# Performance work log

Hardware: AMD Instinct MI355X
Metric: run time of the kernel (lower is better)

Reference implementation:

```python
import jax, jax.numpy as jnp
import numpy as np

NUM_CLASSES = 20
EPS = 1e-10


def setup_inputs() -> dict:
    key = jax.random.key(0)
    k1, k2 = jax.random.split(key)
    shape = (2, 128, 256, 256)
    prediction = jax.random.randint(k1, shape, 0, NUM_CLASSES, dtype=jnp.int32)
    target = jax.random.randint(k2, shape, 0, NUM_CLASSES, dtype=jnp.int32)
    return {"prediction": prediction, "target": target}


def reference(prediction, target):
    C = NUM_CLASSES
    pred = prediction.reshape(-1)
    tgt = target.reshape(-1)
    # Per-class voxel counts in a single histogram pass each.
    pred_cnt = jnp.bincount(pred, length=C).astype(jnp.float32)  # tp + fp per class
    tgt_cnt = jnp.bincount(tgt, length=C).astype(jnp.float32)    # tp + fn per class
    # tp: voxels where pred == tgt, binned by class (mismatches routed to bin C).
    tp = jnp.bincount(jnp.where(pred == tgt, pred, C), length=C + 1)[:C].astype(jnp.float32)
    # dsc = 2tp / (2tp + fp + fn + eps); fp = pred_cnt - tp, fn = tgt_cnt - tp.
    # Classes absent from both tensors give 0/eps = 0, matching the original's
    # skip-then-zero behavior.
    dscs = 2.0 * tp / (pred_cnt + tgt_cnt + EPS)
    return jnp.mean(dscs[1:])
```

## Files before the change

### kernel.cpp

```cpp
#include <hip/hip_runtime.h>

#define NC 20
#define THREADS 256
#define BLOCKS 2048
#define GRAN 8
#define EPSF 1e-10f

typedef unsigned long long u64;
typedef unsigned int u32;

#define PART_OFF 64
#define WS_NEEDED (256 + 30 * BLOCKS * 4)

static __device__ __forceinline__ void pair_update(int p, int t,
                                                   u64& np, u64& nt, u64& ne)
{
    u64 ip = 1ull << (3 * p);
    u64 it = 1ull << (3 * t);
    np += ip;
    nt += it;
    ne += (p == t) ? ip : 0ull;
}

__global__ __launch_bounds__(THREADS) void dice_slice(
    const int* __restrict__ pred, const int* __restrict__ tgt,
    u32* __restrict__ part)
{
    constexpr u64 M = 0x01C71C71C71C71C7ull;
    __shared__ u32 swave[4][30];
    const int tid = threadIdx.x;
    const int g   = blockIdx.x * THREADS + tid;
    const int S   = BLOCKS * THREADS;
    const int4* p4 = (const int4*)pred;
    const int4* t4 = (const int4*)tgt;

    u64 aeP=0, aoP=0, aeT=0, aoT=0, aeE=0, aoE=0;

    #pragma unroll
    for (int k = 0; k < GRAN; ++k) {
        int4 P = p4[g + k * S];
        int4 T = t4[g + k * S];
        u64 np = 0, nt = 0, ne = 0;
        pair_update(P.x, T.x, np, nt, ne);
        pair_update(P.y, T.y, np, nt, ne);
        pair_update(P.z, T.z, np, nt, ne);
        pair_update(P.w, T.w, np, nt, ne);
        aeP += np & M;        aoP += (np >> 3) & M;
        aeT += nt & M;        aoT += (nt >> 3) & M;
        aeE += ne & M;        aoE += (ne >> 3) & M;
    }

    const int wid  = tid >> 6;
    const int lane = tid & 63;
    #pragma unroll
    for (int j = 0; j < 10; ++j) {
        const int sh = 6 * j;
        u32 sP = (u32)((aeP >> sh) & 63) | ((u32)((aoP >> sh) & 63) << 16);
        u32 sT = (u32)((aeT >> sh) & 63) | ((u32)((aoT >> sh) & 63) << 16);
        u32 sE = (u32)((aeE >> sh) & 63) | ((u32)((aoE >> sh) & 63) << 16);
        #pragma unroll
        for (int d = 32; d >= 1; d >>= 1) {
            sP += __shfl_down(sP, d, 64);
            sT += __shfl_down(sT, d, 64);
            sE += __shfl_down(sE, d, 64);
        }
        if (lane == 0) {
            swave[wid][j]      = sP;
            swave[wid][10 + j] = sT;
            swave[wid][20 + j] = sE;
        }
    }
    __syncthreads();

    if (tid < 30) {
        u32 s = swave[0][tid] + swave[1][tid] + swave[2][tid] + swave[3][tid];
        part[tid * BLOCKS + blockIdx.x] = s;
    }
}

__global__ __launch_bounds__(THREADS) void dice_reduce(
    const u32* __restrict__ part, u32* __restrict__ gc)
{
    __shared__ u32 sw[2][4];
    const int j    = blockIdx.x;
    const int tid  = threadIdx.x;
    const int wid  = tid >> 6;
    const int lane = tid & 63;
    u32 lo = 0, hi = 0;
    #pragma unroll
    for (int k = 0; k < BLOCKS / THREADS; ++k) {
        u32 v = part[j * BLOCKS + tid + k * THREADS];
        lo += v & 0xFFFFu;
        hi += v >> 16;
    }
    #pragma unroll
    for (int d = 32; d >= 1; d >>= 1) {
        lo += __shfl_down(lo, d, 64);
        hi += __shfl_down(hi, d, 64);
    }
    if (lane == 0) { sw[0][wid] = lo; sw[1][wid] = hi; }
    __syncthreads();
    if (tid == 0) {
        lo = sw[0][0] + sw[0][1] + sw[0][2] + sw[0][3];
        hi = sw[1][0] + sw[1][1] + sw[1][2] + sw[1][3];
        const int hist = j / 10;
        const int k2   = j % 10;
        gc[hist * NC + 2 * k2]     = lo;
        gc[hist * NC + 2 * k2 + 1] = hi;
    }
}

__global__ __launch_bounds__(THREADS) void dice_joint(
    const int* __restrict__ pred, const int* __restrict__ tgt,
    u32* __restrict__ gc, long long n4)
{
    __shared__ u32 h[4 * NC * NC];
    const int tid = threadIdx.x;
    for (int k = tid; k < 4 * NC * NC; k += THREADS) h[k] = 0u;
    __syncthreads();
    u32* hw = &h[(tid >> 6) * NC * NC];
    const int4* p4 = (const int4*)pred;
    const int4* t4 = (const int4*)tgt;
    const long long stride = (long long)2048 * THREADS;
    for (long long i = (long long)blockIdx.x * THREADS + tid; i < n4; i += stride) {
        int4 P = p4[i];
        int4 T = t4[i];
        atomicAdd(&hw[P.x * NC + T.x], 1u);
        atomicAdd(&hw[P.y * NC + T.y], 1u);
        atomicAdd(&hw[P.z * NC + T.z], 1u);
        atomicAdd(&hw[P.w * NC + T.w], 1u);
    }
    __syncthreads();
    for (int k = tid; k < NC * NC; k += THREADS)
        h[k] = h[k] + h[NC*NC + k] + h[2*NC*NC + k] + h[3*NC*NC + k];
    __syncthreads();
    if (tid < 3 * (NC - 1)) {
        const int which = tid / (NC - 1);
        const int c     = tid % (NC - 1) + 1;
        u32 s = 0;
        if (which == 0)      { for (int t = 0; t < NC; ++t) s += h[c * NC + t]; }
        else if (which == 1) { for (int p = 0; p < NC; ++p) s += h[p * NC + c]; }
        else                 { s = h[c * NC + c]; }
        atomicAdd(&gc[which * NC + c], s);
    }
}

__global__ void dice_final(const u32* __restrict__ gc, float* __restrict__ out)
{
    const int c = threadIdx.x;
    float contrib = 0.0f;
    if (c >= 1 && c < NC) {
        float pc = (float)gc[c];
        float tc = (float)gc[NC + c];
        float tp = (float)gc[2 * NC + c];
        contrib = 2.0f * tp / (pc + tc + EPSF);
    }
    #pragma unroll
    for (int d = 32; d >= 1; d >>= 1) contrib += __shfl_down(contrib, d, 64);
    if (c == 0) out[0] = contrib * (1.0f / 19.0f);
}

extern "C" void kernel_launch(void* const* d_in, const int* in_sizes, int n_in,
                              void* d_out, int out_size, void* d_ws, size_t ws_size,
                              hipStream_t stream) {
    const int* pred = (const int*)d_in[0];
    const int* tgt  = (const int*)d_in[1];
    u32* gc   = (u32*)d_ws;
    u32* part = (u32*)d_ws + PART_OFF;

    const int n  = in_sizes[0];
    const int n4 = n >> 2;

    if (n4 == BLOCKS * THREADS * GRAN && ws_size >= (size_t)WS_NEEDED) {
        dice_slice<<<BLOCKS, THREADS, 0, stream>>>(pred, tgt, part);
        dice_reduce<<<30, THREADS, 0, stream>>>(part, gc);
    } else {
        hipMemsetAsync(d_ws, 0, 3 * NC * sizeof(u32), stream);
        dice_joint<<<2048, THREADS, 0, stream>>>(pred, tgt, gc, (long long)n4);
    }
    dice_final<<<1, 64, 0, stream>>>(gc, (float*)d_out);
}
```

Before: 39.55 us.

## Prefetch all granules via inline asm loads and fuse reduce with final kernel

The slice kernel now issues all 16 vector loads up front with inline global_load_dwordx4 and consumes each granule after a matching s_waitcnt, so memory latency overlaps with the bit-packed counting. The separate 30-block reduce kernel and the final dice kernel are merged into a single 1024-thread block that reduces the partials and computes the mean dice. This removes one kernel launch and the global round-trip through the workspace. The hand-written waitcnt counts depend on the compiler not issuing other vector memory ops in between, which is fragile.

```diff
diff --git a/kernel.cpp b/kernel.cpp
--- a/kernel.cpp
+++ b/kernel.cpp
@@ -8,6 +8,7 @@
 
 typedef unsigned long long u64;
 typedef unsigned int u32;
+typedef int v4i __attribute__((ext_vector_type(4)));
 
 #define PART_OFF 64
 #define WS_NEEDED (256 + 30 * BLOCKS * 4)
@@ -29,26 +30,39 @@
     constexpr u64 M = 0x01C71C71C71C71C7ull;
     __shared__ u32 swave[4][30];
     const int tid = threadIdx.x;
-    const int g   = blockIdx.x * THREADS + tid;
-    const int S   = BLOCKS * THREADS;
-    const int4* p4 = (const int4*)pred;
-    const int4* t4 = (const int4*)tgt;
-
-    u64 aeP=0, aoP=0, aeT=0, aoT=0, aeE=0, aoE=0;
-
+    const long long g = (long long)blockIdx.x * THREADS + tid;
+    const u64 SB = (u64)BLOCKS * THREADS * 16ull;
+
+    u64 baseP = (u64)pred + (u64)g * 16ull;
+    u64 baseT = (u64)tgt  + (u64)g * 16ull;
+
+    v4i P[GRAN], T[GRAN];
     #pragma unroll
     for (int k = 0; k < GRAN; ++k) {
-        int4 P = p4[g + k * S];
-        int4 T = t4[g + k * S];
-        u64 np = 0, nt = 0, ne = 0;
-        pair_update(P.x, T.x, np, nt, ne);
-        pair_update(P.y, T.y, np, nt, ne);
-        pair_update(P.z, T.z, np, nt, ne);
-        pair_update(P.w, T.w, np, nt, ne);
-        aeP += np & M;        aoP += (np >> 3) & M;
-        aeT += nt & M;        aoT += (nt >> 3) & M;
-        aeE += ne & M;        aoE += (ne >> 3) & M;
-    }
+        asm volatile("global_load_dwordx4 %0, %2, off\n\t"
+                     "global_load_dwordx4 %1, %3, off"
+                     : "=&v"(P[k]), "=&v"(T[k])
+                     : "v"(baseP + (u64)k * SB), "v"(baseT + (u64)k * SB));
+    }
+
+    u64 aeP=0, aoP=0, aeT=0, aoT=0, aeE=0, aoE=0;
+
+#define GRANULE(K, W)                                                          \
+    do {                                                                       \
+        asm volatile("s_waitcnt vmcnt(" #W ")" : "+v"(P[K]), "+v"(T[K]));      \
+        u64 np = 0, nt = 0, ne = 0;       \
+        pair_update(P[K].x, T[K].x, np, nt, ne);                               \
+        pair_update(P[K].y, T[K].y, np, nt, ne);                               \
+        pair_update(P[K].z, T[K].z, np, nt, ne);                               \
+        pair_update(P[K].w, T[K].w, np, nt, ne);                               \
+        aeP += np & M;        aoP += (np >> 3) & M;                            \
+        aeT += nt & M;        aoT += (nt >> 3) & M;                            \
+        aeE += ne & M;        aoE += (ne >> 3) & M;                            \
+    } while (0)
+
+    GRANULE(0, 14); GRANULE(1, 12); GRANULE(2, 10); GRANULE(3, 8);
+    GRANULE(4, 6);  GRANULE(5, 4);  GRANULE(6, 2);  GRANULE(7, 0);
+#undef GRANULE
 
     const int wid  = tid >> 6;
     const int lane = tid & 63;
@@ -78,35 +92,46 @@
     }
 }
 
-__global__ __launch_bounds__(THREADS) void dice_reduce(
-    const u32* __restrict__ part, u32* __restrict__ gc)
-{
-    __shared__ u32 sw[2][4];
-    const int j    = blockIdx.x;
-    const int tid  = threadIdx.x;
-    const int wid  = tid >> 6;
-    const int lane = tid & 63;
-    u32 lo = 0, hi = 0;
-    #pragma unroll
-    for (int k = 0; k < BLOCKS / THREADS; ++k) {
-        u32 v = part[j * BLOCKS + tid + k * THREADS];
-        lo += v & 0xFFFFu;
-        hi += v >> 16;
-    }
-    #pragma unroll
-    for (int d = 32; d >= 1; d >>= 1) {
-        lo += __shfl_down(lo, d, 64);
-        hi += __shfl_down(hi, d, 64);
-    }
-    if (lane == 0) { sw[0][wid] = lo; sw[1][wid] = hi; }
-    __syncthreads();
-    if (tid == 0) {
-        lo = sw[0][0] + sw[0][1] + sw[0][2] + sw[0][3];
-        hi = sw[1][0] + sw[1][1] + sw[1][2] + sw[1][3];
-        const int hist = j / 10;
-        const int k2   = j % 10;
-        gc[hist * NC + 2 * k2]     = lo;
-        gc[hist * NC + 2 * k2 + 1] = hi;
+__global__ __launch_bounds__(1024) void dice_reduce_final(
+    const u32* __restrict__ part, float* __restrict__ out)
+{
+    __shared__ u32 cls[64];
+    const int tid = threadIdx.x;
+    const int j   = tid >> 5;
+    const int l   = tid & 31;
+    if (j < 30) {
+        const uint4* row = (const uint4*)(part + j * BLOCKS);
+        u32 lo = 0, hi = 0;
+        #pragma unroll
+        for (int i = 0; i < BLOCKS / 128; ++i) {
+            uint4 v = row[l + i * 32];
+            lo += (v.x & 0xFFFFu) + (v.y & 0xFFFFu) + (v.z & 0xFFFFu) + (v.w & 0xFFFFu);
+            hi += (v.x >> 16)     + (v.y >> 16)     + (v.z >> 16)     + (v.w >> 16);
+        }
+        #pragma unroll
+        for (int d = 16; d >= 1; d >>= 1) {
+            lo += __shfl_down(lo, d, 32);
+            hi += __shfl_down(hi, d, 32);
+        }
+        if (l == 0) {
+            const int hist = j / 10, kk = j % 10;
+            cls[hist * NC + 2 * kk]     = lo;
+            cls[hist * NC + 2 * kk + 1] = hi;
+        }
+    }
+    __syncthreads();
+    if (tid < 64) {
+        const int c = tid;
+        float contrib = 0.0f;
+        if (c >= 1 && c < NC) {
+            float pc = (float)cls[c];
+            float tc = (float)cls[NC + c];
+            float tp = (float)cls[2 * NC + c];
+            contrib = 2.0f * tp / (pc + tc + EPSF);
+        }
+        #pragma unroll
+        for (int d = 32; d >= 1; d >>= 1) contrib += __shfl_down(contrib, d, 64);
+        if (tid == 0) out[0] = contrib * (1.0f / 19.0f);
     }
 }
 
@@ -123,12 +148,12 @@
     const int4* t4 = (const int4*)tgt;
     const long long stride = (long long)2048 * THREADS;
     for (long long i = (long long)blockIdx.x * THREADS + tid; i < n4; i += stride) {
-        int4 P = p4[i];
-        int4 T = t4[i];
-        atomicAdd(&hw[P.x * NC + T.x], 1u);
-        atomicAdd(&hw[P.y * NC + T.y], 1u);
-        atomicAdd(&hw[P.z * NC + T.z], 1u);
-        atomicAdd(&hw[P.w * NC + T.w], 1u);
+        int4 Pv = p4[i];
+        int4 Tv = t4[i];
+        atomicAdd(&hw[Pv.x * NC + Tv.x], 1u);
+        atomicAdd(&hw[Pv.y * NC + Tv.y], 1u);
+        atomicAdd(&hw[Pv.z * NC + Tv.z], 1u);
+        atomicAdd(&hw[Pv.w * NC + Tv.w], 1u);
     }
     __syncthreads();
     for (int k = tid; k < NC * NC; k += THREADS)
@@ -173,10 +198,10 @@
 
     if (n4 == BLOCKS * THREADS * GRAN && ws_size >= (size_t)WS_NEEDED) {
         dice_slice<<<BLOCKS, THREADS, 0, stream>>>(pred, tgt, part);
-        dice_reduce<<<30, THREADS, 0, stream>>>(part, gc);
+        dice_reduce_final<<<1, 1024, 0, stream>>>(part, (float*)d_out);
     } else {
-        hipMemsetAsync(d_ws, 0, 3 * NC * sizeof(u32), stream);
+        (void)hipMemsetAsync(d_ws, 0, 3 * NC * sizeof(u32), stream);
         dice_joint<<<2048, THREADS, 0, stream>>>(pred, tgt, gc, (long long)n4);
-    }
-    dice_final<<<1, 64, 0, stream>>>(gc, (float*)d_out);
-}
+        dice_final<<<1, 64, 0, stream>>>(gc, (float*)d_out);
+    }
+}
```

Result: faster. 36.96 us (-6.6%).
